# Kernel optimization log

Hardware: AMD Instinct MI355X
Metric: run time of the kernel (lower is better)

## Reference

```python
import jax, jax.numpy as jnp
import numpy as np

N_NODES = 50000
N_EDGES = 800000
NFEAT = 512
NHID = 128
NCLASS = 40


def setup_inputs() -> dict:
    key = jax.random.key(0)
    ks = jax.random.split(key, 12)
    s = lambda fan_in: 1.0 / np.sqrt(fan_in)
    return {
        "x": jax.random.normal(ks[0], (N_NODES, NFEAT), dtype=jnp.float32),
        "edge_src": jax.random.randint(ks[1], (N_EDGES,), 0, N_NODES, dtype=jnp.int32),
        "edge_dst": jax.random.randint(ks[2], (N_EDGES,), 0, N_NODES, dtype=jnp.int32),
        "edge_val": jax.random.uniform(ks[3], (N_EDGES,), dtype=jnp.float32) * 0.1,
        # GraphConvolution 1: nfeat -> nhid
        "W1": jax.random.uniform(ks[4], (NFEAT, NHID), jnp.float32, -s(NFEAT), s(NFEAT)),
        "b1": jnp.zeros((NHID,), jnp.float32),
        # res1 Linear: nfeat -> nhid (stored as [in, out])
        "Wr1": jax.random.uniform(ks[5], (NFEAT, NHID), jnp.float32, -s(NFEAT), s(NFEAT)),
        "br1": jnp.zeros((NHID,), jnp.float32),
        # GraphConvolution 2: 2*nhid -> nclass
        "W2": jax.random.uniform(ks[6], (2 * NHID, NCLASS), jnp.float32, -s(2 * NHID), s(2 * NHID)),
        "b2": jnp.zeros((NCLASS,), jnp.float32),
        # res2 Linear: 2*nhid -> nclass
        "Wr2": jax.random.uniform(ks[7], (2 * NHID, NCLASS), jnp.float32, -s(2 * NHID), s(2 * NHID)),
        "br2": jnp.zeros((NCLASS,), jnp.float32),
    }


def _spmm(edge_src, edge_dst, edge_val, support):
    # adj @ support with adj in COO form: out[d] += val * support[s]
    msgs = edge_val[:, None] * support[edge_src]  # [E, F] irregular gather
    return jax.ops.segment_sum(msgs, edge_dst, num_segments=N_NODES)


def reference(x, edge_src, edge_dst, edge_val, W1, b1, Wr1, br1, W2, b2, Wr2, br2):
    # gc1(x, adj) = adj @ (x @ W1) + b1
    gc1 = _spmm(edge_src, edge_dst, edge_val, x @ W1) + b1
    h = jnp.concatenate([jax.nn.relu(gc1), x @ Wr1 + br1], axis=1)  # [N, 2*nhid]
    # dropout is identity in eval mode
    gc2 = _spmm(edge_src, edge_dst, edge_val, h @ W2) + b2
    h2 = gc2 + (h @ Wr2 + br2)
    return jax.nn.log_softmax(h2, axis=1)
```

## Files before the change

### kernel.cpp

```cpp
#include <hip/hip_runtime.h>
#include <stdint.h>

#define N_NODES 50000
#define N_EDGES 800000
#define NFEAT 512
#define NHID 128
#define NCLASS 40
#define NB 196

typedef __attribute__((ext_vector_type(8))) __bf16 bf16x8;
typedef __attribute__((ext_vector_type(4))) float f32x4;

__device__ __forceinline__ uint16_t f2b(float f) {
  uint32_t x = __float_as_uint(f);
  uint32_t r = (x + 0x7fffu + ((x >> 16) & 1u)) >> 16;
  return (uint16_t)r;
}
__device__ __forceinline__ float b2f(uint16_t u) {
  return __uint_as_float(((uint32_t)u) << 16);
}

__global__ void k_cast_x(const float* __restrict__ x, uint16_t* __restrict__ xb, int n8) {
  int i = blockIdx.x * blockDim.x + threadIdx.x;
  if (i >= n8) return;
  const float4* p = (const float4*)x + (size_t)i * 2;
  float4 a = p[0], b = p[1];
  union { uint16_t u[8]; uint4 v; } o;
  o.u[0] = f2b(a.x); o.u[1] = f2b(a.y); o.u[2] = f2b(a.z); o.u[3] = f2b(a.w);
  o.u[4] = f2b(b.x); o.u[5] = f2b(b.y); o.u[6] = f2b(b.z); o.u[7] = f2b(b.w);
  ((uint4*)xb)[i] = o.v;
}

__global__ void k_prep_w1(const float* __restrict__ W1, const float* __restrict__ Wr1,
                          uint16_t* __restrict__ WT) {
  int idx = blockIdx.x * 256 + threadIdx.x;
  if (idx >= 256 * 512) return;
  int n = idx >> 9, k = idx & 511;
  float v = (n < 128) ? W1[(size_t)k * 128 + n] : Wr1[(size_t)k * 128 + (n - 128)];
  WT[idx] = f2b(v);
}

__global__ void k_prep_w2(const float* __restrict__ W2, const float* __restrict__ Wr2,
                          uint16_t* __restrict__ WT) {
  int idx = blockIdx.x * 256 + threadIdx.x;
  if (idx >= 128 * 256) return;
  int n = idx >> 8, k = idx & 255;
  float v = 0.f;
  if (n < 40) v = W2[(size_t)k * 40 + n];
  else if (n < 80) v = Wr2[(size_t)k * 40 + (n - 40)];
  WT[idx] = f2b(v);
}

__global__ void k_hist(const int* __restrict__ dst, int* __restrict__ counts) {
  int e = blockIdx.x * 256 + threadIdx.x;
  if (e < N_EDGES) atomicAdd(&counts[dst[e]], 1);
}

__global__ void k_blocksum(const int* __restrict__ counts, int* __restrict__ blocksums) {
  __shared__ int red[256];
  int t = threadIdx.x, idx = blockIdx.x * 256 + t;
  red[t] = (idx < N_NODES) ? counts[idx] : 0;
  __syncthreads();
  for (int o = 128; o; o >>= 1) {
    if (t < o) red[t] += red[t + o];
    __syncthreads();
  }
  if (t == 0) blocksums[blockIdx.x] = red[0];
}

__global__ void k_scan2(const int* __restrict__ counts, const int* __restrict__ blocksums,
                        int* __restrict__ offs) {
  __shared__ int red[256];
  __shared__ int sc[256];
  int b = blockIdx.x, t = threadIdx.x;
  red[t] = (t < b && t < NB) ? blocksums[t] : 0;
  __syncthreads();
  for (int o = 128; o; o >>= 1) {
    if (t < o) red[t] += red[t + o];
    __syncthreads();
  }
  int prefix = red[0];
  int idx = b * 256 + t;
  int c = (idx < N_NODES) ? counts[idx] : 0;
  sc[t] = c;
  __syncthreads();
  for (int o = 1; o < 256; o <<= 1) {
    int v = (t >= o) ? sc[t - o] : 0;
    __syncthreads();
    sc[t] += v;
    __syncthreads();
  }
  if (idx <= N_NODES) offs[idx] = prefix + sc[t] - c;
}

__global__ void k_scatter(const int* __restrict__ src, const int* __restrict__ dst,
                          const float* __restrict__ val, const int* __restrict__ offs,
                          int* __restrict__ cursor, int2* __restrict__ es) {
  int e = blockIdx.x * 256 + threadIdx.x;
  if (e >= N_EDGES) return;
  int d = dst[e];
  int pos = offs[d] + atomicAdd(&cursor[d], 1);
  es[pos] = make_int2(src[e], __float_as_int(val[e]));
}

template <int K, int EPI>
__global__ __launch_bounds__(256, 2) void k_gemm(
    const uint16_t* __restrict__ A, const uint16_t* __restrict__ BT, int M,
    uint16_t* __restrict__ out_bf_a, uint16_t* __restrict__ out_bf_b,
    float* __restrict__ out_f, const float* __restrict__ bias_a,
    const float* __restrict__ bias_b) {
  __shared__ uint16_t Al[128 * 64];
  __shared__ uint16_t Bl[128 * 64];
  const int tid = threadIdx.x;
  const int w = tid >> 6, lane = tid & 63;
  const int wm = w >> 1, wn = w & 1;
  const int m0 = blockIdx.x * 128;
  const int n0 = blockIdx.y * 128;

  f32x4 acc[4][4];
#pragma unroll
  for (int t = 0; t < 4; t++)
#pragma unroll
    for (int u = 0; u < 4; u++) acc[t][u] = (f32x4)0.f;

  const int lrow = lane >> 3;
  const int lcol = lane & 7;

  for (int kb = 0; kb < K / 64; ++kb) {
    __syncthreads();
    const int k0 = kb * 64;
#pragma unroll
    for (int i = 0; i < 4; i++) {
      int rr = (w * 4 + i) * 8 + lrow;
      int ra = m0 + rr;
      if (ra >= M) ra = M - 1;
      const uint16_t* gA = A + (size_t)ra * K + k0 + lcol * 8;
      __builtin_amdgcn_global_load_lds(
          (const __attribute__((address_space(1))) void*)gA,
          (__attribute__((address_space(3))) void*)&Al[(w * 4 + i) * 512], 16, 0, 0);
      int rb = n0 + rr;
      const uint16_t* gB = BT + (size_t)rb * K + k0 + lcol * 8;
      __builtin_amdgcn_global_load_lds(
          (const __attribute__((address_space(1))) void*)gB,
          (__attribute__((address_space(3))) void*)&Bl[(w * 4 + i) * 512], 16, 0, 0);
    }
    __syncthreads();
#pragma unroll
    for (int s = 0; s < 2; s++) {
      bf16x8 av[4], bv[4];
#pragma unroll
      for (int t = 0; t < 4; t++)
        av[t] = *(const bf16x8*)&Al[(wm * 64 + t * 16 + (lane & 15)) * 64 + s * 32 + (lane >> 4) * 8];
#pragma unroll
      for (int u = 0; u < 4; u++)
        bv[u] = *(const bf16x8*)&Bl[(wn * 64 + u * 16 + (lane & 15)) * 64 + s * 32 + (lane >> 4) * 8];
#pragma unroll
      for (int t = 0; t < 4; t++)
#pragma unroll
        for (int u = 0; u < 4; u++)
          acc[t][u] = __builtin_amdgcn_mfma_f32_16x16x32_bf16(av[t], bv[u], acc[t][u], 0, 0, 0);
    }
  }

  const int cl = lane & 15, rq = lane >> 4;
#pragma unroll
  for (int t = 0; t < 4; t++) {
#pragma unroll
    for (int u = 0; u < 4; u++) {
#pragma unroll
      for (int r = 0; r < 4; r++) {
        int m = m0 + wm * 64 + t * 16 + rq * 4 + r;
        int n = n0 + wn * 64 + u * 16 + cl;
        if (m >= M) continue;
        float v = acc[t][u][r];
        if constexpr (EPI == 1) {
          if (n < 128)
            out_bf_a[(size_t)m * 128 + n] = f2b(v);
          else
            out_bf_b[(size_t)m * 256 + n] = f2b(v + bias_a[n - 128]);
        } else {
          if (n < 40)
            out_bf_a[(size_t)m * 40 + n] = f2b(v);
          else if (n < 80)
            out_f[(size_t)m * 40 + (n - 40)] = v + bias_a[n - 40] + bias_b[n - 40];
        }
      }
    }
  }
}

__global__ void k_spmm1_csr(const int* __restrict__ offs, const int2* __restrict__ es,
                            const uint16_t* __restrict__ S1b, const float* __restrict__ b1,
                            uint16_t* __restrict__ h) {
  int node = blockIdx.x * 4 + (threadIdx.x >> 6);
  if (node >= N_NODES) return;
  int lane = threadIdx.x & 63;
  int beg = offs[node], end = offs[node + 1];
  float a0 = 0.f, a1 = 0.f;
  int p = beg;
  for (; p + 4 <= end; p += 4) {
    int2 e0 = es[p], e1 = es[p + 1], e2 = es[p + 2], e3 = es[p + 3];
    uint32_t p0 = *(const uint32_t*)(S1b + (size_t)e0.x * 128 + lane * 2);
    uint32_t p1 = *(const uint32_t*)(S1b + (size_t)e1.x * 128 + lane * 2);
    uint32_t p2 = *(const uint32_t*)(S1b + (size_t)e2.x * 128 + lane * 2);
    uint32_t p3 = *(const uint32_t*)(S1b + (size_t)e3.x * 128 + lane * 2);
    float v0 = __int_as_float(e0.y), v1 = __int_as_float(e1.y);
    float v2 = __int_as_float(e2.y), v3 = __int_as_float(e3.y);
    a0 += v0 * b2f((uint16_t)p0) + v1 * b2f((uint16_t)p1) + v2 * b2f((uint16_t)p2) + v3 * b2f((uint16_t)p3);
    a1 += v0 * b2f((uint16_t)(p0 >> 16)) + v1 * b2f((uint16_t)(p1 >> 16)) +
          v2 * b2f((uint16_t)(p2 >> 16)) + v3 * b2f((uint16_t)(p3 >> 16));
  }
  for (; p < end; p++) {
    int2 ev = es[p];
    float v = __int_as_float(ev.y);
    uint32_t pk = *(const uint32_t*)(S1b + (size_t)ev.x * 128 + lane * 2);
    a0 += v * b2f((uint16_t)pk);
    a1 += v * b2f((uint16_t)(pk >> 16));
  }
  a0 += b1[lane * 2];
  a1 += b1[lane * 2 + 1];
  a0 = a0 > 0.f ? a0 : 0.f;
  a1 = a1 > 0.f ? a1 : 0.f;
  *(uint32_t*)(h + (size_t)node * 256 + lane * 2) = (uint32_t)f2b(a0) | ((uint32_t)f2b(a1) << 16);
}

__global__ void k_spmm2_lsm(const int* __restrict__ offs, const int2* __restrict__ es,
                            const uint16_t* __restrict__ S2b, const float* __restrict__ oacc,
                            float* __restrict__ out) {
  int node = blockIdx.x * 4 + (threadIdx.x >> 6);
  if (node >= N_NODES) return;
  int lane = threadIdx.x & 63;
  int beg = offs[node], end = offs[node + 1];
  float a = 0.f;
  int fl = lane < 40 ? lane : 0;
  int p = beg;
  for (; p + 4 <= end; p += 4) {
    int2 e0 = es[p], e1 = es[p + 1], e2 = es[p + 2], e3 = es[p + 3];
    float x0 = b2f(S2b[(size_t)e0.x * 40 + fl]);
    float x1 = b2f(S2b[(size_t)e1.x * 40 + fl]);
    float x2 = b2f(S2b[(size_t)e2.x * 40 + fl]);
    float x3 = b2f(S2b[(size_t)e3.x * 40 + fl]);
    a += __int_as_float(e0.y) * x0 + __int_as_float(e1.y) * x1 +
         __int_as_float(e2.y) * x2 + __int_as_float(e3.y) * x3;
  }
  for (; p < end; p++) {
    int2 ev = es[p];
    a += __int_as_float(ev.y) * b2f(S2b[(size_t)ev.x * 40 + fl]);
  }
  float val = (lane < 40) ? a + oacc[(size_t)node * 40 + lane] : -1e30f;
  float mv = val;
#pragma unroll
  for (int o = 32; o; o >>= 1) {
    float t = __shfl_xor(mv, o, 64);
    mv = mv > t ? mv : t;
  }
  float e = (lane < 40) ? __expf(val - mv) : 0.f;
  float se = e;
#pragma unroll
  for (int o = 32; o; o >>= 1) se += __shfl_xor(se, o, 64);
  if (lane < 40) out[(size_t)node * 40 + lane] = val - mv - __logf(se);
}

extern "C" void kernel_launch(void* const* d_in, const int* in_sizes, int n_in,
                              void* d_out, int out_size, void* d_ws, size_t ws_size,
                              hipStream_t stream) {
  const float* x = (const float*)d_in[0];
  const int* esrc = (const int*)d_in[1];
  const int* edst = (const int*)d_in[2];
  const float* eval = (const float*)d_in[3];
  const float* W1 = (const float*)d_in[4];
  const float* b1 = (const float*)d_in[5];
  const float* Wr1 = (const float*)d_in[6];
  const float* br1 = (const float*)d_in[7];
  const float* W2 = (const float*)d_in[8];
  const float* b2 = (const float*)d_in[9];
  const float* Wr2 = (const float*)d_in[10];
  const float* br2 = (const float*)d_in[11];
  float* out = (float*)d_out;

  char* ws = (char*)d_ws;
  uint16_t* xb   = (uint16_t*)(ws);
  uint16_t* S1b  = (uint16_t*)(ws + 51200000);
  uint16_t* h    = (uint16_t*)(ws + 64000000);
  uint16_t* WT1  = (uint16_t*)(ws + 89600000);
  uint16_t* WT2  = (uint16_t*)(ws + 89862144);
  uint16_t* S2b  = (uint16_t*)(ws + 89927680);
  float*    oacc = (float*)(ws + 93927680);
  int*      counts = (int*)(ws + 101927680);
  int*      cursor = (int*)(ws + 102127680);
  int*      offs   = (int*)(ws + 102327680);
  int2*     es     = (int2*)(ws + 102527744);
  int*      blocksums = (int*)(ws + 108927744);

  hipMemsetAsync(counts, 0, 400000, stream);

  k_cast_x<<<(3200000 + 255) / 256, 256, 0, stream>>>(x, xb, 3200000);
  k_prep_w1<<<(256 * 512) / 256, 256, 0, stream>>>(W1, Wr1, WT1);
  k_prep_w2<<<(128 * 256) / 256, 256, 0, stream>>>(W2, Wr2, WT2);

  k_hist<<<(N_EDGES + 255) / 256, 256, 0, stream>>>(edst, counts);
  k_blocksum<<<NB, 256, 0, stream>>>(counts, blocksums);
  k_scan2<<<NB, 256, 0, stream>>>(counts, blocksums, offs);
  k_scatter<<<(N_EDGES + 255) / 256, 256, 0, stream>>>(esrc, edst, eval, offs, cursor, es);

  dim3 g1(391, 2);
  k_gemm<512, 1><<<g1, 256, 0, stream>>>(xb, WT1, N_NODES, S1b, h, nullptr, br1, nullptr);

  k_spmm1_csr<<<(N_NODES + 3) / 4, 256, 0, stream>>>(offs, es, S1b, b1, h);

  dim3 g2(391, 1);
  k_gemm<256, 2><<<g2, 256, 0, stream>>>(h, WT2, N_NODES, S2b, nullptr, oacc, b2, br2);

  k_spmm2_lsm<<<(N_NODES + 3) / 4, 256, 0, stream>>>(offs, es, S2b, oacc, out);
}
```

Baseline: 393.2 us.

## Fuse x cast into GEMM1 and vectorize SpMM gathers with padded rows

After: 364.7 us. -7.2%, faster.

```diff
diff --git a/kernel.cpp b/kernel.cpp
--- a/kernel.cpp
+++ b/kernel.cpp
@@ -18,17 +18,6 @@
 }
 __device__ __forceinline__ float b2f(uint16_t u) {
   return __uint_as_float(((uint32_t)u) << 16);
-}
-
-__global__ void k_cast_x(const float* __restrict__ x, uint16_t* __restrict__ xb, int n8) {
-  int i = blockIdx.x * blockDim.x + threadIdx.x;
-  if (i >= n8) return;
-  const float4* p = (const float4*)x + (size_t)i * 2;
-  float4 a = p[0], b = p[1];
-  union { uint16_t u[8]; uint4 v; } o;
-  o.u[0] = f2b(a.x); o.u[1] = f2b(a.y); o.u[2] = f2b(a.z); o.u[3] = f2b(a.w);
-  o.u[4] = f2b(b.x); o.u[5] = f2b(b.y); o.u[6] = f2b(b.z); o.u[7] = f2b(b.w);
-  ((uint4*)xb)[i] = o.v;
 }
 
 __global__ void k_prep_w1(const float* __restrict__ W1, const float* __restrict__ Wr1,
@@ -103,19 +92,100 @@
   es[pos] = make_int2(src[e], __float_as_int(val[e]));
 }
 
-template <int K, int EPI>
-__global__ __launch_bounds__(256, 2) void k_gemm(
+__global__ __launch_bounds__(512) void k_gemm1_fused(
+    const float* __restrict__ x, const uint16_t* __restrict__ BT,
+    uint16_t* __restrict__ S1b, uint16_t* __restrict__ h, const float* __restrict__ br1) {
+  __shared__ uint16_t Al[128 * 72];
+  __shared__ uint16_t Bl[256 * 64];
+  const int tid = threadIdx.x;
+  const int w = tid >> 6, lane = tid & 63;
+  const int wm = w >> 2, wn = w & 3;
+  const int m0 = blockIdx.x * 128;
+  const int M = N_NODES;
+
+  f32x4 acc[4][4];
+#pragma unroll
+  for (int t = 0; t < 4; t++)
+#pragma unroll
+    for (int u = 0; u < 4; u++) acc[t][u] = (f32x4)0.f;
+
+  const int arow = tid >> 2;
+  const int aslot = tid & 3;
+  int ar = m0 + arow;
+  if (ar >= M) ar = M - 1;
+  const float* gxbase = x + (size_t)ar * NFEAT + aslot * 16;
+
+  for (int kb = 0; kb < 8; ++kb) {
+    __syncthreads();
+    const int k0 = kb * 64;
+    {
+      const float4* gp = (const float4*)(gxbase + k0);
+      float4 f0 = gp[0], f1 = gp[1], f2 = gp[2], f3 = gp[3];
+      union { uint16_t u[8]; uint4 v; } o0, o1;
+      o0.u[0] = f2b(f0.x); o0.u[1] = f2b(f0.y); o0.u[2] = f2b(f0.z); o0.u[3] = f2b(f0.w);
+      o0.u[4] = f2b(f1.x); o0.u[5] = f2b(f1.y); o0.u[6] = f2b(f1.z); o0.u[7] = f2b(f1.w);
+      o1.u[0] = f2b(f2.x); o1.u[1] = f2b(f2.y); o1.u[2] = f2b(f2.z); o1.u[3] = f2b(f2.w);
+      o1.u[4] = f2b(f3.x); o1.u[5] = f2b(f3.y); o1.u[6] = f2b(f3.z); o1.u[7] = f2b(f3.w);
+      *(uint4*)&Al[arow * 72 + aslot * 16] = o0.v;
+      *(uint4*)&Al[arow * 72 + aslot * 16 + 8] = o1.v;
+    }
+#pragma unroll
+    for (int i = 0; i < 4; i++) {
+      int chunk = w * 4 + i;
+      const uint16_t* gB = BT + (size_t)(chunk * 8 + (lane >> 3)) * NFEAT + k0 + (lane & 7) * 8;
+      __builtin_amdgcn_global_load_lds(
+          (const __attribute__((address_space(1))) void*)gB,
+          (__attribute__((address_space(3))) void*)&Bl[chunk * 512], 16, 0, 0);
+    }
+    __syncthreads();
+#pragma unroll
+    for (int s = 0; s < 2; s++) {
+      bf16x8 av[4], bv[4];
+#pragma unroll
+      for (int t = 0; t < 4; t++)
+        av[t] = *(const bf16x8*)&Al[(wm * 64 + t * 16 + (lane & 15)) * 72 + s * 32 + (lane >> 4) * 8];
+#pragma unroll
+      for (int u = 0; u < 4; u++)
+        bv[u] = *(const bf16x8*)&Bl[(wn * 64 + u * 16 + (lane & 15)) * 64 + s * 32 + (lane >> 4) * 8];
+#pragma unroll
+      for (int t = 0; t < 4; t++)
+#pragma unroll
+        for (int u = 0; u < 4; u++)
+          acc[t][u] = __builtin_amdgcn_mfma_f32_16x16x32_bf16(av[t], bv[u], acc[t][u], 0, 0, 0);
+    }
+  }
+
+  const int cl = lane & 15, rq = lane >> 4;
+#pragma unroll
+  for (int t = 0; t < 4; t++) {
+#pragma unroll
+    for (int u = 0; u < 4; u++) {
+#pragma unroll
+      for (int r = 0; r < 4; r++) {
+        int m = m0 + wm * 64 + t * 16 + rq * 4 + r;
+        int n = wn * 64 + u * 16 + cl;
+        if (m >= M) continue;
+        float v = acc[t][u][r];
+        if (n < 128)
+          S1b[(size_t)m * 128 + n] = f2b(v);
+        else
+          h[(size_t)m * 256 + n] = f2b(v + br1[n - 128]);
+      }
+    }
+  }
+}
+
+__global__ __launch_bounds__(256, 2) void k_gemm2(
     const uint16_t* __restrict__ A, const uint16_t* __restrict__ BT, int M,
-    uint16_t* __restrict__ out_bf_a, uint16_t* __restrict__ out_bf_b,
-    float* __restrict__ out_f, const float* __restrict__ bias_a,
-    const float* __restrict__ bias_b) {
+    uint16_t* __restrict__ S2b, float* __restrict__ oacc,
+    const float* __restrict__ b2, const float* __restrict__ br2) {
   __shared__ uint16_t Al[128 * 64];
   __shared__ uint16_t Bl[128 * 64];
   const int tid = threadIdx.x;
   const int w = tid >> 6, lane = tid & 63;
   const int wm = w >> 1, wn = w & 1;
   const int m0 = blockIdx.x * 128;
-  const int n0 = blockIdx.y * 128;
+  const int K = 256;
 
   f32x4 acc[4][4];
 #pragma unroll
@@ -138,8 +208,7 @@
       __builtin_amdgcn_global_load_lds(
           (const __attribute__((address_space(1))) void*)gA,
           (__attribute__((address_space(3))) void*)&Al[(w * 4 + i) * 512], 16, 0, 0);
-      int rb = n0 + rr;
-      const uint16_t* gB = BT + (size_t)rb * K + k0 + lcol * 8;
+      const uint16_t* gB = BT + (size_t)rr * K + k0 + lcol * 8;
       __builtin_amdgcn_global_load_lds(
           (const __attribute__((address_space(1))) void*)gB,
           (__attribute__((address_space(3))) void*)&Bl[(w * 4 + i) * 512], 16, 0, 0);
@@ -170,20 +239,13 @@
 #pragma unroll
       for (int r = 0; r < 4; r++) {
         int m = m0 + wm * 64 + t * 16 + rq * 4 + r;
-        int n = n0 + wn * 64 + u * 16 + cl;
+        int n = wn * 64 + u * 16 + cl;
         if (m >= M) continue;
         float v = acc[t][u][r];
-        if constexpr (EPI == 1) {
-          if (n < 128)
-            out_bf_a[(size_t)m * 128 + n] = f2b(v);
-          else
-            out_bf_b[(size_t)m * 256 + n] = f2b(v + bias_a[n - 128]);
-        } else {
-          if (n < 40)
-            out_bf_a[(size_t)m * 40 + n] = f2b(v);
-          else if (n < 80)
-            out_f[(size_t)m * 40 + (n - 40)] = v + bias_a[n - 40] + bias_b[n - 40];
-        }
+        if (n < 40) S2b[(size_t)m * 64 + n] = f2b(v);
+        else if (n < 64) S2b[(size_t)m * 64 + n] = 0;
+        if (n >= 40 && n < 80) oacc[(size_t)m * 64 + (n - 40)] = v + b2[n - 40] + br2[n - 40];
+        else if (n >= 80 && n < 104) oacc[(size_t)m * 64 + (n - 40)] = 0.f;
       }
     }
   }
@@ -195,33 +257,40 @@
   int node = blockIdx.x * 4 + (threadIdx.x >> 6);
   if (node >= N_NODES) return;
   int lane = threadIdx.x & 63;
+  int eg = lane >> 4;
+  int fg = lane & 15;
   int beg = offs[node], end = offs[node + 1];
-  float a0 = 0.f, a1 = 0.f;
-  int p = beg;
-  for (; p + 4 <= end; p += 4) {
-    int2 e0 = es[p], e1 = es[p + 1], e2 = es[p + 2], e3 = es[p + 3];
-    uint32_t p0 = *(const uint32_t*)(S1b + (size_t)e0.x * 128 + lane * 2);
-    uint32_t p1 = *(const uint32_t*)(S1b + (size_t)e1.x * 128 + lane * 2);
-    uint32_t p2 = *(const uint32_t*)(S1b + (size_t)e2.x * 128 + lane * 2);
-    uint32_t p3 = *(const uint32_t*)(S1b + (size_t)e3.x * 128 + lane * 2);
-    float v0 = __int_as_float(e0.y), v1 = __int_as_float(e1.y);
-    float v2 = __int_as_float(e2.y), v3 = __int_as_float(e3.y);
-    a0 += v0 * b2f((uint16_t)p0) + v1 * b2f((uint16_t)p1) + v2 * b2f((uint16_t)p2) + v3 * b2f((uint16_t)p3);
-    a1 += v0 * b2f((uint16_t)(p0 >> 16)) + v1 * b2f((uint16_t)(p1 >> 16)) +
-          v2 * b2f((uint16_t)(p2 >> 16)) + v3 * b2f((uint16_t)(p3 >> 16));
-  }
-  for (; p < end; p++) {
-    int2 ev = es[p];
-    float v = __int_as_float(ev.y);
-    uint32_t pk = *(const uint32_t*)(S1b + (size_t)ev.x * 128 + lane * 2);
-    a0 += v * b2f((uint16_t)pk);
-    a1 += v * b2f((uint16_t)(pk >> 16));
-  }
-  a0 += b1[lane * 2];
-  a1 += b1[lane * 2 + 1];
-  a0 = a0 > 0.f ? a0 : 0.f;
-  a1 = a1 > 0.f ? a1 : 0.f;
-  *(uint32_t*)(h + (size_t)node * 256 + lane * 2) = (uint32_t)f2b(a0) | ((uint32_t)f2b(a1) << 16);
+  float a[8];
+#pragma unroll
+  for (int j = 0; j < 8; j++) a[j] = 0.f;
+  for (int p = beg; p < end; p += 4) {
+    int pe = p + eg;
+    bool ok = pe < end;
+    int2 ev = es[ok ? pe : beg];
+    float v = ok ? __int_as_float(ev.y) : 0.f;
+    uint4 g = *(const uint4*)(S1b + (size_t)ev.x * 128 + fg * 8);
+    a[0] += v * b2f((uint16_t)g.x); a[1] += v * b2f((uint16_t)(g.x >> 16));
+    a[2] += v * b2f((uint16_t)g.y); a[3] += v * b2f((uint16_t)(g.y >> 16));
+    a[4] += v * b2f((uint16_t)g.z); a[5] += v * b2f((uint16_t)(g.z >> 16));
+    a[6] += v * b2f((uint16_t)g.w); a[7] += v * b2f((uint16_t)(g.w >> 16));
+  }
+#pragma unroll
+  for (int j = 0; j < 8; j++) {
+    a[j] += __shfl_xor(a[j], 16, 64);
+    a[j] += __shfl_xor(a[j], 32, 64);
+  }
+  if (eg == 0) {
+    const float4* bp = (const float4*)(b1 + fg * 8);
+    float4 ba = bp[0], bb = bp[1];
+    float r0 = a[0] + ba.x, r1 = a[1] + ba.y, r2 = a[2] + ba.z, r3 = a[3] + ba.w;
+    float r4 = a[4] + bb.x, r5 = a[5] + bb.y, r6 = a[6] + bb.z, r7 = a[7] + bb.w;
+    union { uint16_t u[8]; uint4 v; } o;
+    o.u[0] = f2b(r0 > 0.f ? r0 : 0.f); o.u[1] = f2b(r1 > 0.f ? r1 : 0.f);
+    o.u[2] = f2b(r2 > 0.f ? r2 : 0.f); o.u[3] = f2b(r3 > 0.f ? r3 : 0.f);
+    o.u[4] = f2b(r4 > 0.f ? r4 : 0.f); o.u[5] = f2b(r5 > 0.f ? r5 : 0.f);
+    o.u[6] = f2b(r6 > 0.f ? r6 : 0.f); o.u[7] = f2b(r7 > 0.f ? r7 : 0.f);
+    *(uint4*)(h + (size_t)node * 256 + fg * 8) = o.v;
+  }
 }
 
 __global__ void k_spmm2_lsm(const int* __restrict__ offs, const int2* __restrict__ es,
@@ -230,35 +299,59 @@
   int node = blockIdx.x * 4 + (threadIdx.x >> 6);
   if (node >= N_NODES) return;
   int lane = threadIdx.x & 63;
+  int eg = lane >> 3;
+  int fg = lane & 7;
   int beg = offs[node], end = offs[node + 1];
-  float a = 0.f;
-  int fl = lane < 40 ? lane : 0;
-  int p = beg;
-  for (; p + 4 <= end; p += 4) {
-    int2 e0 = es[p], e1 = es[p + 1], e2 = es[p + 2], e3 = es[p + 3];
-    float x0 = b2f(S2b[(size_t)e0.x * 40 + fl]);
-    float x1 = b2f(S2b[(size_t)e1.x * 40 + fl]);
-    float x2 = b2f(S2b[(size_t)e2.x * 40 + fl]);
-    float x3 = b2f(S2b[(size_t)e3.x * 40 + fl]);
-    a += __int_as_float(e0.y) * x0 + __int_as_float(e1.y) * x1 +
-         __int_as_float(e2.y) * x2 + __int_as_float(e3.y) * x3;
-  }
-  for (; p < end; p++) {
-    int2 ev = es[p];
-    a += __int_as_float(ev.y) * b2f(S2b[(size_t)ev.x * 40 + fl]);
-  }
-  float val = (lane < 40) ? a + oacc[(size_t)node * 40 + lane] : -1e30f;
-  float mv = val;
-#pragma unroll
-  for (int o = 32; o; o >>= 1) {
+  float a[8];
+#pragma unroll
+  for (int j = 0; j < 8; j++) a[j] = 0.f;
+  for (int p = beg; p < end; p += 8) {
+    int pe = p + eg;
+    bool ok = pe < end;
+    int2 ev = es[ok ? pe : beg];
+    float v = ok ? __int_as_float(ev.y) : 0.f;
+    uint4 g = *(const uint4*)(S2b + (size_t)ev.x * 64 + fg * 8);
+    a[0] += v * b2f((uint16_t)g.x); a[1] += v * b2f((uint16_t)(g.x >> 16));
+    a[2] += v * b2f((uint16_t)g.y); a[3] += v * b2f((uint16_t)(g.y >> 16));
+    a[4] += v * b2f((uint16_t)g.z); a[5] += v * b2f((uint16_t)(g.z >> 16));
+    a[6] += v * b2f((uint16_t)g.w); a[7] += v * b2f((uint16_t)(g.w >> 16));
+  }
+#pragma unroll
+  for (int j = 0; j < 8; j++) {
+    a[j] += __shfl_xor(a[j], 8, 64);
+    a[j] += __shfl_xor(a[j], 16, 64);
+    a[j] += __shfl_xor(a[j], 32, 64);
+  }
+  const float4* op = (const float4*)(oacc + (size_t)node * 64 + fg * 8);
+  float4 o0 = op[0], o1 = op[1];
+  float v0 = a[0] + o0.x, v1 = a[1] + o0.y, v2 = a[2] + o0.z, v3 = a[3] + o0.w;
+  float v4 = a[4] + o1.x, v5 = a[5] + o1.y, v6 = a[6] + o1.z, v7 = a[7] + o1.w;
+  bool valid = fg < 5;
+  float m01 = v0 > v1 ? v0 : v1, m23 = v2 > v3 ? v2 : v3;
+  float m45 = v4 > v5 ? v4 : v5, m67 = v6 > v7 ? v6 : v7;
+  float ml = m01 > m23 ? m01 : m23;
+  float mh = m45 > m67 ? m45 : m67;
+  float mv = ml > mh ? ml : mh;
+  mv = valid ? mv : -1e30f;
+#pragma unroll
+  for (int o = 1; o <= 4; o <<= 1) {
     float t = __shfl_xor(mv, o, 64);
     mv = mv > t ? mv : t;
   }
-  float e = (lane < 40) ? __expf(val - mv) : 0.f;
-  float se = e;
-#pragma unroll
-  for (int o = 32; o; o >>= 1) se += __shfl_xor(se, o, 64);
-  if (lane < 40) out[(size_t)node * 40 + lane] = val - mv - __logf(se);
+  float se = 0.f;
+  if (valid)
+    se = __expf(v0 - mv) + __expf(v1 - mv) + __expf(v2 - mv) + __expf(v3 - mv) +
+         __expf(v4 - mv) + __expf(v5 - mv) + __expf(v6 - mv) + __expf(v7 - mv);
+#pragma unroll
+  for (int o = 1; o <= 4; o <<= 1) se += __shfl_xor(se, o, 64);
+  if (eg == 0 && valid) {
+    float ls = mv + __logf(se);
+    float4 r0 = make_float4(v0 - ls, v1 - ls, v2 - ls, v3 - ls);
+    float4 r1 = make_float4(v4 - ls, v5 - ls, v6 - ls, v7 - ls);
+    float4* wp = (float4*)(out + (size_t)node * 40 + fg * 8);
+    wp[0] = r0;
+    wp[1] = r1;
+  }
 }
 
 extern "C" void kernel_launch(void* const* d_in, const int* in_sizes, int n_in,
@@ -279,22 +372,20 @@
   float* out = (float*)d_out;
 
   char* ws = (char*)d_ws;
-  uint16_t* xb   = (uint16_t*)(ws);
-  uint16_t* S1b  = (uint16_t*)(ws + 51200000);
-  uint16_t* h    = (uint16_t*)(ws + 64000000);
-  uint16_t* WT1  = (uint16_t*)(ws + 89600000);
-  uint16_t* WT2  = (uint16_t*)(ws + 89862144);
-  uint16_t* S2b  = (uint16_t*)(ws + 89927680);
-  float*    oacc = (float*)(ws + 93927680);
-  int*      counts = (int*)(ws + 101927680);
-  int*      cursor = (int*)(ws + 102127680);
-  int*      offs   = (int*)(ws + 102327680);
-  int2*     es     = (int2*)(ws + 102527744);
-  int*      blocksums = (int*)(ws + 108927744);
+  uint16_t* S1b  = (uint16_t*)(ws);
+  uint16_t* h    = (uint16_t*)(ws + 12800000);
+  uint16_t* WT1  = (uint16_t*)(ws + 38400000);
+  uint16_t* WT2  = (uint16_t*)(ws + 38662144);
+  uint16_t* S2b  = (uint16_t*)(ws + 38727680);
+  float*    oacc = (float*)(ws + 45127680);
+  int*      counts = (int*)(ws + 57927680);
+  int*      cursor = (int*)(ws + 58127680);
+  int*      offs   = (int*)(ws + 58327680);
+  int2*     es     = (int2*)(ws + 58527744);
+  int*      blocksums = (int*)(ws + 64927744);
 
   hipMemsetAsync(counts, 0, 400000, stream);
 
-  k_cast_x<<<(3200000 + 255) / 256, 256, 0, stream>>>(x, xb, 3200000);
   k_prep_w1<<<(256 * 512) / 256, 256, 0, stream>>>(W1, Wr1, WT1);
   k_prep_w2<<<(128 * 256) / 256, 256, 0, stream>>>(W2, Wr2, WT2);
 
@@ -303,13 +394,11 @@
   k_scan2<<<NB, 256, 0, stream>>>(counts, blocksums, offs);
   k_scatter<<<(N_EDGES + 255) / 256, 256, 0, stream>>>(esrc, edst, eval, offs, cursor, es);
 
-  dim3 g1(391, 2);
-  k_gemm<512, 1><<<g1, 256, 0, stream>>>(xb, WT1, N_NODES, S1b, h, nullptr, br1, nullptr);
+  k_gemm1_fused<<<391, 512, 0, stream>>>(x, WT1, S1b, h, br1);
 
   k_spmm1_csr<<<(N_NODES + 3) / 4, 256, 0, stream>>>(offs, es, S1b, b1, h);
 
-  dim3 g2(391, 1);
-  k_gemm<256, 2><<<g2, 256, 0, stream>>>(h, WT2, N_NODES, S2b, nullptr, oacc, b2, br2);
+  k_gemm2<<<391, 256, 0, stream>>>(h, WT2, N_NODES, S2b, oacc, b2, br2);
 
   k_spmm2_lsm<<<(N_NODES + 3) / 4, 256, 0, stream>>>(offs, es, S2b, oacc, out);
 }
```
